# Kernel optimization log

Measured on AMD Instinct MI355X. Metric: run time of the kernel, lower is better.

## Reference

```python
import jax, jax.numpy as jnp
import numpy as np

B, T, DIM = 4, 4096, 1024
HEADS, DIM_HEAD = 16, 64
INNER = HEADS * DIM_HEAD
SCALE = DIM_HEAD ** -0.5


def setup_inputs() -> dict:
    key = jax.random.key(0)
    k1, k2, k3, k4 = jax.random.split(key, 4)
    x = jax.random.normal(k1, (B, T, DIM), dtype=jnp.float32)
    mask = jax.random.bernoulli(k2, 0.2, (B, T))  # True = padding
    W_qkv = jax.random.normal(k3, (DIM, 3 * INNER), dtype=jnp.float32) * (DIM ** -0.5)
    W_out = jax.random.normal(k4, (INNER, DIM), dtype=jnp.float32) * (INNER ** -0.5)
    b_out = jnp.zeros((DIM,), dtype=jnp.float32)
    return {"x": x, "mask": mask, "W_qkv": W_qkv, "W_out": W_out, "b_out": b_out}


def reference(x, mask, W_qkv, W_out, b_out):
    Bs, Ts, _ = x.shape
    qkv = x @ W_qkv                                       # [B,T,3*inner]
    q, k, v = jnp.split(qkv, 3, axis=-1)
    # [B,T,H,Dh] -> [B,H,T,Dh]
    reshape = lambda t: t.reshape(Bs, Ts, HEADS, DIM_HEAD).transpose(0, 2, 1, 3)
    q, k, v = reshape(q), reshape(k), reshape(v)
    q = q * SCALE
    k = jax.nn.softmax(k, axis=-2)                        # softmax over sequence dim
    # zero out padded positions AFTER softmax (faithful to original)
    k = jnp.where(mask[:, None, :, None], 0.0, k)
    context = jnp.einsum('bhnd,bhne->bhde', k, v)         # [B,H,Dh,Dh]
    out = jnp.einsum('bhnd,bhde->bhne', q, context)       # [B,H,T,Dh]
    out = out.transpose(0, 2, 1, 3).reshape(Bs, Ts, INNER)
    return out @ W_out + b_out                            # dropout: eval mode (identity)
```

## Files before the change

kernel.cpp:

```cpp
#include <hip/hip_runtime.h>
#include <math.h>


typedef __bf16 bf16;
typedef __attribute__((ext_vector_type(4))) float f32x4;
typedef __attribute__((ext_vector_type(8))) __bf16 bf16x8;
typedef __attribute__((ext_vector_type(4))) __bf16 bf16x4;

#define SCALE_ 0.125f

__device__ __forceinline__ void g2l16(const void* g, void* l) {
  __builtin_amdgcn_global_load_lds((const __attribute__((address_space(1))) void*)g,
                                   (__attribute__((address_space(3))) void*)l, 16, 0, 0);
}

__global__ __launch_bounds__(256) void k_cvt(const float* __restrict__ in,
                                             bf16* __restrict__ out, int n4) {
  int i = blockIdx.x * 256 + threadIdx.x;
  if (i >= n4) return;
  f32x4 v = ((const f32x4*)in)[i];
  bf16x4 o;
  o[0] = (bf16)v[0]; o[1] = (bf16)v[1]; o[2] = (bf16)v[2]; o[3] = (bf16)v[3];
  ((bf16x4*)out)[i] = o;
}

__global__ __launch_bounds__(256) void k_trans(const float* __restrict__ W,
                                               bf16* __restrict__ Wt) {
  __shared__ float t[32][33];
  int n0 = blockIdx.x * 32, k0 = blockIdx.y * 32;
  int tx = threadIdx.x & 31, ty = threadIdx.x >> 5;
  #pragma unroll
  for (int s = 0; s < 4; s++) {
    int k = ty + s * 8;
    t[k][tx] = W[(size_t)(k0 + k) * 3072 + 1024 + n0 + tx];
  }
  __syncthreads();
  #pragma unroll
  for (int s = 0; s < 4; s++) {
    int n = ty + s * 8;
    Wt[(size_t)(n0 + n) * 1024 + k0 + tx] = (bf16)t[tx][n];
  }
}

__global__ __launch_bounds__(256) void k_wq(const float* __restrict__ W,
                                            bf16* __restrict__ wqs) {
  int idx = blockIdx.x * 256 + threadIdx.x;
  int i = idx >> 8, d4 = idx & 255;
  f32x4 v = *(const f32x4*)(W + (size_t)i * 3072 + d4 * 4);
  bf16x4 o;
  o[0] = (bf16)(v[0] * SCALE_); o[1] = (bf16)(v[1] * SCALE_);
  o[2] = (bf16)(v[2] * SCALE_); o[3] = (bf16)(v[3] * SCALE_);
  *(bf16x4*)(wqs + (size_t)i * 1024 + d4 * 4) = o;
}

__global__ __launch_bounds__(256) void k_gemm1(const bf16* __restrict__ A,
                                               const bf16* __restrict__ Bt,
                                               bf16* __restrict__ kv) {
  __shared__ __align__(16) bf16 As[128 * 32];
  __shared__ __align__(16) bf16 Bs[128 * 32];
  const int tid = threadIdx.x;
  const int wave = tid >> 6, lane = tid & 63, l16 = lane & 15, quad = lane >> 4;
  const int wm = (wave >> 1) << 6, wn = (wave & 1) << 6;
  const int row0 = blockIdx.y << 7, col0 = blockIdx.x << 7;
  f32x4 acc[4][4] = {};
  for (int kt = 0; kt < 1024; kt += 32) {
    #pragma unroll
    for (int it = 0; it < 2; ++it) {
      const int cb = (wave * 2 + it) * 64;
      const int c = cb + lane;
      const int m = c >> 2, k8 = (c & 3) * 8;
      g2l16(A  + (size_t)(row0 + m) * 1024 + kt + k8, As + cb * 8);
      g2l16(Bt + (size_t)(col0 + m) * 1024 + kt + k8, Bs + cb * 8);
    }
    __syncthreads();
    bf16x8 af[4], bfr[4];
    #pragma unroll
    for (int i = 0; i < 4; i++) af[i]  = *(const bf16x8*)(As + (wm + i * 16 + l16) * 32 + quad * 8);
    #pragma unroll
    for (int j = 0; j < 4; j++) bfr[j] = *(const bf16x8*)(Bs + (wn + j * 16 + l16) * 32 + quad * 8);
    #pragma unroll
    for (int i = 0; i < 4; i++)
      #pragma unroll
      for (int j = 0; j < 4; j++)
        acc[i][j] = __builtin_amdgcn_mfma_f32_16x16x32_bf16(af[i], bfr[j], acc[i][j], 0, 0, 0);
    __syncthreads();
  }
  #pragma unroll
  for (int i = 0; i < 4; i++) {
    const int gm0 = row0 + wm + i * 16 + quad * 4;
    #pragma unroll
    for (int j = 0; j < 4; j++) {
      const int gc = col0 + wn + j * 16 + l16;
      #pragma unroll
      for (int r = 0; r < 4; r++)
        kv[(size_t)(gm0 + r) * 2048 + gc] = (bf16)acc[i][j][r];
    }
  }
}

__global__ __launch_bounds__(256) void k_stats(const bf16* __restrict__ kv,
                                               float* __restrict__ sumexp) {
  const int b = blockIdx.y, ns = blockIdx.x;
  const int cg = threadIdx.x & 127, half = threadIdx.x >> 7;
  const int n0 = ns * 256 + half * 128;
  float s[8] = {};
  const bf16* p = kv + (size_t)(b * 4096 + n0) * 2048 + cg * 8;
  for (int i = 0; i < 128; i++) {
    bf16x8 t8 = *(const bf16x8*)(p + (size_t)i * 2048);
    #pragma unroll
    for (int j = 0; j < 8; j++) s[j] += __expf((float)t8[j]);
  }
  #pragma unroll
  for (int j = 0; j < 8; j++) atomicAdd(&sumexp[b * 1024 + cg * 8 + j], s[j]);
}

__global__ __launch_bounds__(256) void k_ctx(const bf16* __restrict__ kv,
                                             const int* __restrict__ mask,
                                             float* __restrict__ ctx) {
  __shared__ float Lk[64][68];
  __shared__ float Lv[64][68];
  const int b = blockIdx.z, h = blockIdx.y, ns = blockIdx.x;
  const int tid = threadIdx.x, wave = tid >> 6, lane = tid & 63;
  const int d0 = (lane & 7) * 8, e0 = (lane >> 3) * 8;
  float acc[8][8] = {};
  const int nbase = ns * 512;
  for (int ch = 0; ch < 8; ++ch) {
    const int n0 = nbase + ch * 64;
    __syncthreads();
    #pragma unroll
    for (int it = 0; it < 2; ++it) {
      const int idx = it * 256 + tid;
      const int row = idx >> 3, g = idx & 7;
      const int gn = b * 4096 + n0 + row;
      const float m = mask[gn] ? 0.f : 1.f;
      bf16x8 t8 = *(const bf16x8*)(kv + (size_t)gn * 2048 + h * 64 + g * 8);
      f32x4 lo, hi;
      lo[0] = __expf((float)t8[0]) * m; lo[1] = __expf((float)t8[1]) * m;
      lo[2] = __expf((float)t8[2]) * m; lo[3] = __expf((float)t8[3]) * m;
      hi[0] = __expf((float)t8[4]) * m; hi[1] = __expf((float)t8[5]) * m;
      hi[2] = __expf((float)t8[6]) * m; hi[3] = __expf((float)t8[7]) * m;
      *(f32x4*)&Lk[row][g * 8] = lo;
      *(f32x4*)&Lk[row][g * 8 + 4] = hi;
    }
    #pragma unroll
    for (int it = 0; it < 2; ++it) {
      const int idx = it * 256 + tid;
      const int row = idx >> 3, g = idx & 7;
      const int gn = b * 4096 + n0 + row;
      bf16x8 t8 = *(const bf16x8*)(kv + (size_t)gn * 2048 + 1024 + h * 64 + g * 8);
      f32x4 lo, hi;
      lo[0] = (float)t8[0]; lo[1] = (float)t8[1]; lo[2] = (float)t8[2]; lo[3] = (float)t8[3];
      hi[0] = (float)t8[4]; hi[1] = (float)t8[5]; hi[2] = (float)t8[6]; hi[3] = (float)t8[7];
      *(f32x4*)&Lv[row][g * 8] = lo;
      *(f32x4*)&Lv[row][g * 8 + 4] = hi;
    }
    __syncthreads();
    #pragma unroll 4
    for (int t = 0; t < 16; t++) {
      const int n = (wave << 4) + t;
      f32x4 ka = *(const f32x4*)&Lk[n][d0];
      f32x4 kb = *(const f32x4*)&Lk[n][d0 + 4];
      f32x4 va = *(const f32x4*)&Lv[n][e0];
      f32x4 vb = *(const f32x4*)&Lv[n][e0 + 4];
      float kk[8] = {ka[0], ka[1], ka[2], ka[3], kb[0], kb[1], kb[2], kb[3]};
      float vv[8] = {va[0], va[1], va[2], va[3], vb[0], vb[1], vb[2], vb[3]};
      #pragma unroll
      for (int a = 0; a < 8; a++)
        #pragma unroll
        for (int c = 0; c < 8; c++) acc[a][c] += kk[a] * vv[c];
    }
  }
  __syncthreads();
  float* r0 = &Lk[0][0];
  float* r1 = &Lv[0][0];
  if (wave < 2) {
    float* r = wave ? r1 : r0;
    #pragma unroll
    for (int a = 0; a < 8; a++)
      #pragma unroll
      for (int c = 0; c < 8; c++) r[(d0 + a) * 64 + e0 + c] = acc[a][c];
  }
  __syncthreads();
  if (wave >= 2) {
    float* r = (wave == 3) ? r1 : r0;
    #pragma unroll
    for (int a = 0; a < 8; a++)
      #pragma unroll
      for (int c = 0; c < 8; c++) r[(d0 + a) * 64 + e0 + c] += acc[a][c];
  }
  __syncthreads();
  float* cbase = ctx + ((size_t)(b * 16 + h) << 12);
  for (int i = tid; i < 4096; i += 256) atomicAdd(cbase + i, r0[i] + r1[i]);
}

__global__ __launch_bounds__(256) void k_m2(const float* __restrict__ ctx,
                                            const float* __restrict__ sumexp,
                                            const float* __restrict__ Wout,
                                            bf16* __restrict__ M2t) {
  __shared__ float Lc[64][64];
  __shared__ float Linv[64];
  const int b = blockIdx.z, h = blockIdx.y, jt = blockIdx.x;
  const int tid = threadIdx.x, dg = tid >> 6, jl = tid & 63;
  const float* cbase = ctx + ((size_t)(b * 16 + h) << 12);
  for (int i = tid; i < 4096; i += 256) (&Lc[0][0])[i] = cbase[i];
  if (tid < 64) Linv[tid] = 1.f / sumexp[b * 1024 + h * 64 + tid];
  __syncthreads();
  float acc[4][16] = {};
  const int j0 = jt * 256 + jl;
  for (int e = 0; e < 64; e++) {
    const float* wrow = Wout + (size_t)(h * 64 + e) * 1024 + j0;
    float w0 = wrow[0], w1 = wrow[64], w2 = wrow[128], w3 = wrow[192];
    #pragma unroll
    for (int dd = 0; dd < 16; dd++) {
      float c = Lc[dg * 16 + dd][e];
      acc[0][dd] += c * w0; acc[1][dd] += c * w1;
      acc[2][dd] += c * w2; acc[3][dd] += c * w3;
    }
  }
  #pragma unroll
  for (int jj = 0; jj < 4; jj++) {
    const size_t jrow = ((size_t)b << 20) + (size_t)(jt * 256 + jl + jj * 64) * 1024 + h * 64 + dg * 16;
    #pragma unroll
    for (int dd = 0; dd < 16; dd++)
      M2t[jrow + dd] = (bf16)(acc[jj][dd] * Linv[dg * 16 + dd]);
  }
}

__global__ __launch_bounds__(256) void k_m3(const bf16* __restrict__ M2t,
                                            const bf16* __restrict__ wqs,
                                            bf16* __restrict__ M3t) {
  __shared__ __align__(16) bf16 As[128 * 32];
  __shared__ __align__(16) bf16 Bs[128 * 32];
  const int tid = threadIdx.x;
  const int wave = tid >> 6, lane = tid & 63, l16 = lane & 15, quad = lane >> 4;
  const int wm = (wave >> 1) << 6, wn = (wave & 1) << 6;
  const int row0 = blockIdx.y << 7, col0 = blockIdx.x << 7;
  const bf16* A  = M2t + ((size_t)blockIdx.z << 20);
  bf16*       C  = M3t + ((size_t)blockIdx.z << 20);
  f32x4 acc[4][4] = {};
  for (int kt = 0; kt < 1024; kt += 32) {
    #pragma unroll
    for (int it = 0; it < 2; ++it) {
      const int cb = (wave * 2 + it) * 64;
      const int c = cb + lane;
      const int m = c >> 2, k8 = (c & 3) * 8;
      g2l16(A   + (size_t)(row0 + m) * 1024 + kt + k8, As + cb * 8);
      g2l16(wqs + (size_t)(col0 + m) * 1024 + kt + k8, Bs + cb * 8);
    }
    __syncthreads();
    bf16x8 af[4], bfr[4];
    #pragma unroll
    for (int i = 0; i < 4; i++) af[i]  = *(const bf16x8*)(As + (wm + i * 16 + l16) * 32 + quad * 8);
    #pragma unroll
    for (int j = 0; j < 4; j++) bfr[j] = *(const bf16x8*)(Bs + (wn + j * 16 + l16) * 32 + quad * 8);
    #pragma unroll
    for (int i = 0; i < 4; i++)
      #pragma unroll
      for (int j = 0; j < 4; j++)
        acc[i][j] = __builtin_amdgcn_mfma_f32_16x16x32_bf16(af[i], bfr[j], acc[i][j], 0, 0, 0);
    __syncthreads();
  }
  #pragma unroll
  for (int i = 0; i < 4; i++) {
    const int gm0 = row0 + wm + i * 16 + quad * 4;
    #pragma unroll
    for (int j = 0; j < 4; j++) {
      const int gc = col0 + wn + j * 16 + l16;
      #pragma unroll
      for (int r = 0; r < 4; r++)
        C[(size_t)(gm0 + r) * 1024 + gc] = (bf16)acc[i][j][r];
    }
  }
}

__global__ __launch_bounds__(256) void k_gemm2(const bf16* __restrict__ A,
                                               const bf16* __restrict__ M3t,
                                               const float* __restrict__ bias,
                                               float* __restrict__ out) {
  __shared__ __align__(16) bf16 As[128 * 32];
  __shared__ __align__(16) bf16 Bs[128 * 32];
  const int tid = threadIdx.x;
  const int wave = tid >> 6, lane = tid & 63, l16 = lane & 15, quad = lane >> 4;
  const int wm = (wave >> 1) << 6, wn = (wave & 1) << 6;
  const int row0 = blockIdx.y << 7, col0 = blockIdx.x << 7;
  const bf16* Bt = M3t + ((size_t)(row0 >> 12) << 20);
  f32x4 acc[4][4] = {};
  for (int kt = 0; kt < 1024; kt += 32) {
    #pragma unroll
    for (int it = 0; it < 2; ++it) {
      const int cb = (wave * 2 + it) * 64;
      const int c = cb + lane;
      const int m = c >> 2, k8 = (c & 3) * 8;
      g2l16(A  + (size_t)(row0 + m) * 1024 + kt + k8, As + cb * 8);
      g2l16(Bt + (size_t)(col0 + m) * 1024 + kt + k8, Bs + cb * 8);
    }
    __syncthreads();
    bf16x8 af[4], bfr[4];
    #pragma unroll
    for (int i = 0; i < 4; i++) af[i]  = *(const bf16x8*)(As + (wm + i * 16 + l16) * 32 + quad * 8);
    #pragma unroll
    for (int j = 0; j < 4; j++) bfr[j] = *(const bf16x8*)(Bs + (wn + j * 16 + l16) * 32 + quad * 8);
    #pragma unroll
    for (int i = 0; i < 4; i++)
      #pragma unroll
      for (int j = 0; j < 4; j++)
        acc[i][j] = __builtin_amdgcn_mfma_f32_16x16x32_bf16(af[i], bfr[j], acc[i][j], 0, 0, 0);
    __syncthreads();
  }
  float bj[4];
  #pragma unroll
  for (int j = 0; j < 4; j++) bj[j] = bias[col0 + wn + j * 16 + l16];
  #pragma unroll
  for (int i = 0; i < 4; i++) {
    const int gm0 = row0 + wm + i * 16 + quad * 4;
    #pragma unroll
    for (int j = 0; j < 4; j++) {
      const int gc = col0 + wn + j * 16 + l16;
      #pragma unroll
      for (int r = 0; r < 4; r++)
        out[(size_t)(gm0 + r) * 1024 + gc] = acc[i][j][r] + bj[j];
    }
  }
}

extern "C" void kernel_launch(void* const* d_in, const int* in_sizes, int n_in,
                              void* d_out, int out_size, void* d_ws, size_t ws_size,
                              hipStream_t stream) {
  const float* x    = (const float*)d_in[0];
  const int*   mask = (const int*)d_in[1];
  const float* Wqkv = (const float*)d_in[2];
  const float* Wout = (const float*)d_in[3];
  const float* bout = (const float*)d_in[4];
  float* out = (float*)d_out;
  char* ws = (char*)d_ws;
  bf16*  xb     = (bf16*)(ws);
  bf16*  wt     = (bf16*)(ws + 33554432);
  bf16*  wqs    = (bf16*)(ws + 37748736);
  bf16*  kv     = (bf16*)(ws + 39845888);
  float* sumexp = (float*)(ws + 106954752);
  float* ctx    = (float*)(ws + 106971136);
  bf16*  m2t    = (bf16*)(ws + 108019712);
  bf16*  m3t    = (bf16*)(ws + 116408320);

  hipMemsetAsync(sumexp, 0, 16384 + 1048576, stream);
  k_cvt  <<<16384, 256, 0, stream>>>(x, xb, 4194304);
  k_trans<<<dim3(64, 32), 256, 0, stream>>>(Wqkv, wt);
  k_wq   <<<1024, 256, 0, stream>>>(Wqkv, wqs);
  k_gemm1<<<dim3(16, 128), 256, 0, stream>>>(xb, wt, kv);
  k_stats<<<dim3(16, 4), 256, 0, stream>>>(kv, sumexp);
  k_ctx  <<<dim3(8, 16, 4), 256, 0, stream>>>(kv, mask, ctx);
  k_m2   <<<dim3(4, 16, 4), 256, 0, stream>>>(ctx, sumexp, Wout, m2t);
  k_m3   <<<dim3(8, 8, 4), 256, 0, stream>>>(m2t, wqs, m3t);
  k_gemm2<<<dim3(8, 128), 256, 0, stream>>>(xb, m3t, bout, out);
}
```

Measured before the change: 398.0 us.

## Fuse softmax denominator into context kernel and remap GEMM blocks per XCD

Removes the separate k_stats pass by accumulating the unmasked exp sums for each column inside k_ctx, reducing them through shared memory and one atomic per column per block. This drops a full extra read of the K half of the kv buffer and one kernel launch. Both GEMMs switch to a flat 1D grid whose block index is remapped so consecutive blocks on the same XCD cover adjacent row tiles, aiming for better L2 reuse. k_ctx also moves to a flat grid decoded into batch, head and sequence-chunk indices.

```diff
diff --git a/kernel.cpp b/kernel.cpp
--- a/kernel.cpp
+++ b/kernel.cpp
@@ -61,7 +61,9 @@
   const int tid = threadIdx.x;
   const int wave = tid >> 6, lane = tid & 63, l16 = lane & 15, quad = lane >> 4;
   const int wm = (wave >> 1) << 6, wn = (wave & 1) << 6;
-  const int row0 = blockIdx.y << 7, col0 = blockIdx.x << 7;
+  const int f = blockIdx.x, xcd = f & 7, w = f >> 3;
+  const int row0 = (xcd * 16 + (w >> 4)) << 7;
+  const int col0 = (w & 15) << 7;
   f32x4 acc[4][4] = {};
   for (int kt = 0; kt < 1024; kt += 32) {
     #pragma unroll
@@ -98,31 +100,20 @@
   }
 }
 
-__global__ __launch_bounds__(256) void k_stats(const bf16* __restrict__ kv,
-                                               float* __restrict__ sumexp) {
-  const int b = blockIdx.y, ns = blockIdx.x;
-  const int cg = threadIdx.x & 127, half = threadIdx.x >> 7;
-  const int n0 = ns * 256 + half * 128;
-  float s[8] = {};
-  const bf16* p = kv + (size_t)(b * 4096 + n0) * 2048 + cg * 8;
-  for (int i = 0; i < 128; i++) {
-    bf16x8 t8 = *(const bf16x8*)(p + (size_t)i * 2048);
-    #pragma unroll
-    for (int j = 0; j < 8; j++) s[j] += __expf((float)t8[j]);
-  }
-  #pragma unroll
-  for (int j = 0; j < 8; j++) atomicAdd(&sumexp[b * 1024 + cg * 8 + j], s[j]);
-}
-
 __global__ __launch_bounds__(256) void k_ctx(const bf16* __restrict__ kv,
                                              const int* __restrict__ mask,
+                                             float* __restrict__ sumexp,
                                              float* __restrict__ ctx) {
   __shared__ float Lk[64][68];
   __shared__ float Lv[64][68];
-  const int b = blockIdx.z, h = blockIdx.y, ns = blockIdx.x;
-  const int tid = threadIdx.x, wave = tid >> 6, lane = tid & 63;
+  __shared__ float Sst[64][33];
+  const int blk = blockIdx.x, tid = threadIdx.x;
+  const int wave = tid >> 6, lane = tid & 63;
+  const int ns = blk & 7, h = (blk >> 3) & 15, b = blk >> 7;
   const int d0 = (lane & 7) * 8, e0 = (lane >> 3) * 8;
+  const int g = tid & 7;
   float acc[8][8] = {};
+  float sum8[8] = {};
   const int nbase = ns * 512;
   for (int ch = 0; ch < 8; ++ch) {
     const int n0 = nbase + ch * 64;
@@ -130,22 +121,23 @@
     #pragma unroll
     for (int it = 0; it < 2; ++it) {
       const int idx = it * 256 + tid;
-      const int row = idx >> 3, g = idx & 7;
+      const int row = idx >> 3;
       const int gn = b * 4096 + n0 + row;
       const float m = mask[gn] ? 0.f : 1.f;
       bf16x8 t8 = *(const bf16x8*)(kv + (size_t)gn * 2048 + h * 64 + g * 8);
+      float e[8];
+      #pragma unroll
+      for (int j = 0; j < 8; j++) { e[j] = __expf((float)t8[j]); sum8[j] += e[j]; }
       f32x4 lo, hi;
-      lo[0] = __expf((float)t8[0]) * m; lo[1] = __expf((float)t8[1]) * m;
-      lo[2] = __expf((float)t8[2]) * m; lo[3] = __expf((float)t8[3]) * m;
-      hi[0] = __expf((float)t8[4]) * m; hi[1] = __expf((float)t8[5]) * m;
-      hi[2] = __expf((float)t8[6]) * m; hi[3] = __expf((float)t8[7]) * m;
+      lo[0] = e[0] * m; lo[1] = e[1] * m; lo[2] = e[2] * m; lo[3] = e[3] * m;
+      hi[0] = e[4] * m; hi[1] = e[5] * m; hi[2] = e[6] * m; hi[3] = e[7] * m;
       *(f32x4*)&Lk[row][g * 8] = lo;
       *(f32x4*)&Lk[row][g * 8 + 4] = hi;
     }
     #pragma unroll
     for (int it = 0; it < 2; ++it) {
       const int idx = it * 256 + tid;
-      const int row = idx >> 3, g = idx & 7;
+      const int row = idx >> 3;
       const int gn = b * 4096 + n0 + row;
       bf16x8 t8 = *(const bf16x8*)(kv + (size_t)gn * 2048 + 1024 + h * 64 + g * 8);
       f32x4 lo, hi;
@@ -180,6 +172,11 @@
       #pragma unroll
       for (int c = 0; c < 8; c++) r[(d0 + a) * 64 + e0 + c] = acc[a][c];
   }
+  {
+    const int rg = tid >> 3;
+    #pragma unroll
+    for (int j = 0; j < 8; j++) Sst[g * 8 + j][rg] = sum8[j];
+  }
   __syncthreads();
   if (wave >= 2) {
     float* r = (wave == 3) ? r1 : r0;
@@ -187,6 +184,11 @@
     for (int a = 0; a < 8; a++)
       #pragma unroll
       for (int c = 0; c < 8; c++) r[(d0 + a) * 64 + e0 + c] += acc[a][c];
+  } else if (tid < 64) {
+    float s = 0.f;
+    #pragma unroll 8
+    for (int rg = 0; rg < 32; rg++) s += Sst[tid][rg];
+    atomicAdd(&sumexp[b * 1024 + h * 64 + tid], s);
   }
   __syncthreads();
   float* cbase = ctx + ((size_t)(b * 16 + h) << 12);
@@ -282,7 +284,9 @@
   const int tid = threadIdx.x;
   const int wave = tid >> 6, lane = tid & 63, l16 = lane & 15, quad = lane >> 4;
   const int wm = (wave >> 1) << 6, wn = (wave & 1) << 6;
-  const int row0 = blockIdx.y << 7, col0 = blockIdx.x << 7;
+  const int f = blockIdx.x, xcd = f & 7, w = f >> 3;
+  const int row0 = (xcd * 16 + (w >> 3)) << 7;
+  const int col0 = (w & 7) << 7;
   const bf16* Bt = M3t + ((size_t)(row0 >> 12) << 20);
   f32x4 acc[4][4] = {};
   for (int kt = 0; kt < 1024; kt += 32) {
@@ -346,10 +350,9 @@
   k_cvt  <<<16384, 256, 0, stream>>>(x, xb, 4194304);
   k_trans<<<dim3(64, 32), 256, 0, stream>>>(Wqkv, wt);
   k_wq   <<<1024, 256, 0, stream>>>(Wqkv, wqs);
-  k_gemm1<<<dim3(16, 128), 256, 0, stream>>>(xb, wt, kv);
-  k_stats<<<dim3(16, 4), 256, 0, stream>>>(kv, sumexp);
-  k_ctx  <<<dim3(8, 16, 4), 256, 0, stream>>>(kv, mask, ctx);
+  k_gemm1<<<2048, 256, 0, stream>>>(xb, wt, kv);
+  k_ctx  <<<512, 256, 0, stream>>>(kv, mask, sumexp, ctx);
   k_m2   <<<dim3(4, 16, 4), 256, 0, stream>>>(ctx, sumexp, Wout, m2t);
   k_m3   <<<dim3(8, 8, 4), 256, 0, stream>>>(m2t, wqs, m3t);
-  k_gemm2<<<dim3(8, 128), 256, 0, stream>>>(xb, m3t, bout, out);
-}
+  k_gemm2<<<1024, 256, 0, stream>>>(xb, m3t, bout, out);
+}
```

After: 349.2 us. -12.3%, faster.
